# Optimization experiments

Hardware: AMD Instinct MI355X
Metric: run time of the kernel (lower is better)

## Reference

```python
import jax, jax.numpy as jnp
import numpy as np

B, T, E, R, A, M = 64, 2000, 512, 1024, 512, 8


def setup_inputs() -> dict:
    key = jax.random.key(0)
    ks = jax.random.split(key, 9)
    attention_hidden_state = jax.random.normal(ks[0], (B, R), dtype=jnp.float32)
    memory = jax.random.normal(ks[1], (B, T, E), dtype=jnp.float32)
    previous_location = jax.random.uniform(ks[2], (B, 1, M), dtype=jnp.float32) * 10.0
    mask = jnp.zeros((B, T), dtype=bool)
    # F = Linear(R->A, bias, xavier tanh) -> Linear(A->A, no bias, xavier tanh) -> tanh -> lin(A->3M, bias)
    g = 5.0 / 3.0  # tanh gain
    lim1 = g * np.sqrt(6.0 / (R + A))
    W1 = jax.random.uniform(ks[3], (A, R), minval=-lim1, maxval=lim1, dtype=jnp.float32)
    b1 = jnp.zeros((A,), dtype=jnp.float32)
    lim2 = g * np.sqrt(6.0 / (A + A))
    W2 = jax.random.uniform(ks[4], (A, A), minval=-lim2, maxval=lim2, dtype=jnp.float32)
    lim3 = np.sqrt(1.0 / A)
    Wlin = jax.random.uniform(ks[5], (3 * M, A), minval=-lim3, maxval=lim3, dtype=jnp.float32) * 0.01
    blin = jax.random.uniform(ks[6], (3 * M,), minval=-lim3, maxval=lim3, dtype=jnp.float32) * 0.008 - 2.0
    return {"attention_hidden_state": attention_hidden_state, "memory": memory,
            "previous_location": previous_location, "mask": mask,
            "W1": W1, "b1": b1, "W2": W2, "Wlin": Wlin, "blin": blin}


def reference(attention_hidden_state, memory, previous_location, mask, W1, b1, W2, Wlin, blin):
    # normalize_attention_input=True
    h = jnp.tanh(attention_hidden_state)                       # (B, R)
    x = jnp.tanh((h @ W1.T + b1) @ W2.T)                       # (B, A) 2-layer variant
    y = (x @ Wlin.T + blin)[:, None, :]                        # (B, 1, 3M)
    m = y.shape[-1] // 3
    w, delta, scale = y[..., :m], y[..., m:2 * m], y[..., 2 * m:]
    delta = jax.nn.sigmoid(delta)                              # (B, 1, M)
    loc = previous_location + delta                            # (B, 1, M)
    scale = jax.nn.sigmoid(scale) * 2.0 + 1.0                  # (B, 1, M)
    pos = jnp.arange(memory.shape[1], dtype=memory.dtype)[None, :, None]  # (1, T, 1)
    d = loc - pos                                              # (B, T, M)
    z = 0.5 * (jax.lax.erf((d + 0.5) * scale) - jax.lax.erf((d - 0.5) * scale))
    wmix = jax.nn.sigmoid(w)[:, 0, :]                          # (B, M)
    alignment = jnp.einsum('btm,bm->bt', z, wmix)              # (B, T)
    alignment = jnp.where(mask, jnp.zeros((), alignment.dtype), alignment)  # score_mask_value=0
    attention_weights = jax.nn.softmax(alignment, axis=1)      # (B, T)
    attention_context = jnp.einsum('bt,bte->be', attention_weights, memory)  # (B, E)
    return attention_context, attention_weights, loc
```

## Files before the change

### kernel.cpp

```cpp
#include <hip/hip_runtime.h>
#include <math.h>

#define B 64
#define T 2000
#define E 512
#define R 1024
#define A 512
#define M 8

#define NCH 16
#define TCH (T / NCH)
#define NP  (NCH * 4)

typedef float nfloat4 __attribute__((ext_vector_type(4)));

__device__ __forceinline__ float sigmoidf_(float x) { return 1.0f / (1.0f + expf(-x)); }
__device__ __forceinline__ float dot4_(float4 a, float4 b) {
    return (a.x * b.x + a.y * b.y) + (a.z * b.z + a.w * b.w);
}

__global__ __launch_bounds__(512) void mlp_align_kernel(
    const float* __restrict__ ahs, const float* __restrict__ prev_loc,
    const unsigned char* __restrict__ mask,
    const float* __restrict__ W1, const float* __restrict__ b1,
    const float* __restrict__ W2, const float* __restrict__ Wlin,
    const float* __restrict__ blin,
    float* __restrict__ out_w,
    float* __restrict__ out_loc)
{
    __shared__ float sh_h[R];
    __shared__ float sh_t[A];
    __shared__ float sh_x[A];
    __shared__ float sh_y[3 * M];
    __shared__ float sh_wmix[M], sh_loc[M], sh_scale[M];
    __shared__ float sred[8];
    __shared__ float sbval;

    const int b = blockIdx.x;
    const int tid = threadIdx.x;
    const int wave = tid >> 6;
    const int lane = tid & 63;

    for (int k = tid; k < R; k += 512) sh_h[k] = tanhf(ahs[b * R + k]);
    __syncthreads();

    {
        const float4* h4 = (const float4*)sh_h;
        const float4 h0 = h4[lane], h1 = h4[lane + 64],
                     h2 = h4[lane + 128], h3 = h4[lane + 192];
        for (int j = 0; j < 64; j += 2) {
            const int ja = wave * 64 + j;
            const int jb = ja + 1;
            const float4* ra = (const float4*)(W1 + (size_t)ja * R);
            const float4* rb = (const float4*)(W1 + (size_t)jb * R);
            float4 a0 = ra[lane], a1 = ra[lane + 64], a2 = ra[lane + 128], a3 = ra[lane + 192];
            float4 c0 = rb[lane], c1 = rb[lane + 64], c2 = rb[lane + 128], c3 = rb[lane + 192];
            float accA = (dot4_(h0, a0) + dot4_(h1, a1)) + (dot4_(h2, a2) + dot4_(h3, a3));
            float accB = (dot4_(h0, c0) + dot4_(h1, c1)) + (dot4_(h2, c2) + dot4_(h3, c3));
#pragma unroll
            for (int off = 32; off > 0; off >>= 1) {
                accA += __shfl_down(accA, off);
                accB += __shfl_down(accB, off);
            }
            if (lane == 0) {
                sh_t[ja] = accA + b1[ja];
                sh_t[jb] = accB + b1[jb];
            }
        }
    }
    __syncthreads();

    {
        const float4* t4 = (const float4*)sh_t;
        const float4 t0 = t4[lane], t1 = t4[lane + 64];
        for (int j = 0; j < 64; j += 2) {
            const int ja = wave * 64 + j;
            const int jb = ja + 1;
            const float4* ra = (const float4*)(W2 + (size_t)ja * A);
            const float4* rb = (const float4*)(W2 + (size_t)jb * A);
            float4 a0 = ra[lane], a1 = ra[lane + 64];
            float4 c0 = rb[lane], c1 = rb[lane + 64];
            float accA = dot4_(t0, a0) + dot4_(t1, a1);
            float accB = dot4_(t0, c0) + dot4_(t1, c1);
#pragma unroll
            for (int off = 32; off > 0; off >>= 1) {
                accA += __shfl_down(accA, off);
                accB += __shfl_down(accB, off);
            }
            if (lane == 0) {
                sh_x[ja] = tanhf(accA);
                sh_x[jb] = tanhf(accB);
            }
        }
    }
    __syncthreads();

    if (tid < 16 * 3 * M) {
        const int i = tid >> 4;
        const int l16 = tid & 15;
        float s = 0.f;
        for (int k = l16; k < A; k += 16) s += sh_x[k] * Wlin[i * A + k];
        s += __shfl_down(s, 8, 16);
        s += __shfl_down(s, 4, 16);
        s += __shfl_down(s, 2, 16);
        s += __shfl_down(s, 1, 16);
        if (l16 == 0) sh_y[i] = s + blin[i];
    }
    __syncthreads();

    if (tid < M) {
        const int m = tid;
        const float delta = sigmoidf_(sh_y[M + m]);
        const float loc = prev_loc[b * M + m] + delta;
        sh_wmix[m]  = sigmoidf_(sh_y[m]);
        sh_loc[m]   = loc;
        sh_scale[m] = sigmoidf_(sh_y[2 * M + m]) * 2.0f + 1.0f;
        out_loc[b * M + m] = loc;
    }
    __syncthreads();

    float a[4];
    float lsum = 0.f;
#pragma unroll
    for (int i = 0; i < 4; ++i) {
        const int t = tid + i * 512;
        if (t < T) {
            const float tf = (float)t;
            float v = 0.f;
#pragma unroll
            for (int m = 0; m < M; ++m) {
                const float d = sh_loc[m] - tf;
                const float s = sh_scale[m];
                v += 0.5f * (erff((d + 0.5f) * s) - erff((d - 0.5f) * s)) * sh_wmix[m];
            }
            if (mask[b * T + t]) v = 0.f;
            a[i] = expf(v);
            lsum += a[i];
        } else {
            a[i] = 0.f;
        }
    }
#pragma unroll
    for (int off = 32; off > 0; off >>= 1) lsum += __shfl_down(lsum, off);
    if (lane == 0) sred[wave] = lsum;
    __syncthreads();
    if (tid == 0) {
        float s0 = 0.f;
        for (int i = 0; i < 8; ++i) s0 += sred[i];
        sbval = s0;
    }
    __syncthreads();
    const float inv = 1.0f / sbval;

#pragma unroll
    for (int i = 0; i < 4; ++i) {
        const int t = tid + i * 512;
        if (t < T) out_w[b * T + t] = a[i] * inv;
    }
}

__global__ __launch_bounds__(512) void context_partial_kernel(
    const float* __restrict__ memory,
    const float* __restrict__ w,
    float* __restrict__ partials)
{
    __shared__ float sh_w[TCH];

    const int b = blockIdx.x;
    const int chunk = blockIdx.y;
    const int tid = threadIdx.x;
    const int t0 = chunk * TCH;

    if (tid < TCH) sh_w[tid] = w[b * T + t0 + tid];
    __syncthreads();

    const int e4 = tid & 127;
    const int tp = tid >> 7;
    const nfloat4* mem4 = (const nfloat4*)(memory + (size_t)(b * T + t0) * E);

    float acc0 = 0.f, acc1 = 0.f, acc2 = 0.f, acc3 = 0.f;
#pragma unroll 4
    for (int t = tp; t < TCH; t += 4) {
        const float wv = sh_w[t];
        const nfloat4 mv = __builtin_nontemporal_load(&mem4[(size_t)t * (E / 4) + e4]);
        acc0 += wv * mv.x;
        acc1 += wv * mv.y;
        acc2 += wv * mv.z;
        acc3 += wv * mv.w;
    }

    nfloat4 accv = {acc0, acc1, acc2, acc3};
    nfloat4* dst = (nfloat4*)(partials + (((size_t)b * NCH + chunk) * 4 + tp) * E);
    dst[e4] = accv;
}

__global__ __launch_bounds__(256) void context_reduce_kernel(
    const float* __restrict__ partials,
    float* __restrict__ out_ctx)
{
    const int idx = blockIdx.x * 256 + threadIdx.x;
    const int b = idx >> 7;
    const int e4 = idx & 127;
    const float4* p = (const float4*)partials + (size_t)b * NP * (E / 4) + e4;
    float4 s = {0.f, 0.f, 0.f, 0.f};
#pragma unroll 8
    for (int c = 0; c < NP; ++c) {
        const float4 v = p[(size_t)c * (E / 4)];
        s.x += v.x; s.y += v.y; s.z += v.z; s.w += v.w;
    }
    ((float4*)out_ctx)[idx] = s;
}

extern "C" void kernel_launch(void* const* d_in, const int* in_sizes, int n_in,
                              void* d_out, int out_size, void* d_ws, size_t ws_size,
                              hipStream_t stream) {
    const float* ahs      = (const float*)d_in[0];
    const float* memory   = (const float*)d_in[1];
    const float* prev_loc = (const float*)d_in[2];
    const unsigned char* mask = (const unsigned char*)d_in[3];
    const float* W1   = (const float*)d_in[4];
    const float* b1   = (const float*)d_in[5];
    const float* W2   = (const float*)d_in[6];
    const float* Wlin = (const float*)d_in[7];
    const float* blin = (const float*)d_in[8];

    float* out = (float*)d_out;
    float* out_ctx = out;
    float* out_w   = out + B * E;
    float* out_loc = out + B * E + B * T;
    float* partials = (float*)d_ws;

    mlp_align_kernel<<<dim3(B), dim3(512), 0, stream>>>(
        ahs, prev_loc, mask, W1, b1, W2, Wlin, blin, out_w, out_loc);

    context_partial_kernel<<<dim3(B, NCH), dim3(512), 0, stream>>>(
        memory, out_w, partials);

    context_reduce_kernel<<<dim3((B * E / 4) / 256), dim3(256), 0, stream>>>(
        partials, out_ctx);
}
```

Before: 434.3 us.

## Split MLP into batched layer kernels that reuse weight rows across four batches

The single per-batch MLP+alignment kernel is split into separate layer1, layer2 and head/alignment kernels. The layer kernels process four batch rows per block over a 16x8 grid, so each W1/W2 row is loaded once per four batches and the work is spread over more blocks. Wave reductions now use DPP instructions instead of shuffles. This cuts the redundant per-batch weight traffic (W1 is 2 MB) and improves parallelism, at the cost of two extra kernel launches and workspace round trips.

```diff
diff --git a/kernel.cpp b/kernel.cpp
--- a/kernel.cpp
+++ b/kernel.cpp
@@ -19,92 +19,143 @@
     return (a.x * b.x + a.y * b.y) + (a.z * b.z + a.w * b.w);
 }
 
-__global__ __launch_bounds__(512) void mlp_align_kernel(
-    const float* __restrict__ ahs, const float* __restrict__ prev_loc,
+__device__ __forceinline__ float wave_sum64_(float v) {
+#define DPPA_(c) v += __int_as_float(__builtin_amdgcn_update_dpp(0, __float_as_int(v), c, 0xf, 0xf, false))
+    DPPA_(0x111);
+    DPPA_(0x112);
+    DPPA_(0x114);
+    DPPA_(0x118);
+    DPPA_(0x142);
+    DPPA_(0x143);
+#undef DPPA_
+    return __int_as_float(__builtin_amdgcn_readlane(__float_as_int(v), 63));
+}
+
+__global__ __launch_bounds__(512) void layer1_kernel(
+    const float* __restrict__ ahs, const float* __restrict__ W1,
+    const float* __restrict__ b1, float* __restrict__ tws)
+{
+    __shared__ float4 sh_h[4 * 256];
+
+    const int bq = blockIdx.x, jt = blockIdx.y;
+    const int tid = threadIdx.x;
+    const int wave = tid >> 6, lane = tid & 63;
+    const int b0 = bq * 4;
+
+#pragma unroll
+    for (int s = 0; s < 2; ++s) {
+        const int idx = tid + s * 512;
+        const int bb = idx >> 8, k4 = idx & 255;
+        float4 v = ((const float4*)(ahs + (size_t)(b0 + bb) * R))[k4];
+        v.x = tanhf(v.x); v.y = tanhf(v.y); v.z = tanhf(v.z); v.w = tanhf(v.w);
+        sh_h[idx] = v;
+    }
+    __syncthreads();
+
+    float4 h4[4][4];
+#pragma unroll
+    for (int bb = 0; bb < 4; ++bb)
+#pragma unroll
+        for (int p = 0; p < 4; ++p)
+            h4[bb][p] = sh_h[bb * 256 + p * 64 + lane];
+
+    const int jbase = jt * 64 + wave * 8;
+#pragma unroll
+    for (int jj = 0; jj < 8; ++jj) {
+        const int j = jbase + jj;
+        const float4* wr = (const float4*)(W1 + (size_t)j * R);
+        const float4 w0 = wr[lane], w1 = wr[64 + lane],
+                     w2 = wr[128 + lane], w3 = wr[192 + lane];
+        const float bias = b1[j];
+        float r[4];
+#pragma unroll
+        for (int bb = 0; bb < 4; ++bb) {
+            float acc = (dot4_(h4[bb][0], w0) + dot4_(h4[bb][1], w1)) +
+                        (dot4_(h4[bb][2], w2) + dot4_(h4[bb][3], w3));
+            r[bb] = wave_sum64_(acc);
+        }
+        if (lane == 0) {
+#pragma unroll
+            for (int bb = 0; bb < 4; ++bb)
+                tws[(size_t)(b0 + bb) * A + j] = r[bb] + bias;
+        }
+    }
+}
+
+__global__ __launch_bounds__(512) void layer2_kernel(
+    const float* __restrict__ tws, const float* __restrict__ W2,
+    float* __restrict__ xws)
+{
+    __shared__ float4 sh_t[4 * 128];
+
+    const int bq = blockIdx.x, jt = blockIdx.y;
+    const int tid = threadIdx.x;
+    const int wave = tid >> 6, lane = tid & 63;
+    const int b0 = bq * 4;
+
+    {
+        const int bb = tid >> 7, k4 = tid & 127;
+        sh_t[tid] = ((const float4*)(tws + (size_t)(b0 + bb) * A))[k4];
+    }
+    __syncthreads();
+
+    float4 t4[4][2];
+#pragma unroll
+    for (int bb = 0; bb < 4; ++bb)
+#pragma unroll
+        for (int p = 0; p < 2; ++p)
+            t4[bb][p] = sh_t[bb * 128 + p * 64 + lane];
+
+    const int jbase = jt * 64 + wave * 8;
+#pragma unroll
+    for (int jj = 0; jj < 8; ++jj) {
+        const int j = jbase + jj;
+        const float4* wr = (const float4*)(W2 + (size_t)j * A);
+        const float4 w0 = wr[lane], w1 = wr[64 + lane];
+        float r[4];
+#pragma unroll
+        for (int bb = 0; bb < 4; ++bb) {
+            float acc = dot4_(t4[bb][0], w0) + dot4_(t4[bb][1], w1);
+            r[bb] = wave_sum64_(acc);
+        }
+        if (lane == 0) {
+#pragma unroll
+            for (int bb = 0; bb < 4; ++bb)
+                xws[(size_t)(b0 + bb) * A + j] = tanhf(r[bb]);
+        }
+    }
+}
+
+__global__ __launch_bounds__(256) void head_align_kernel(
+    const float* __restrict__ xws, const float* __restrict__ prev_loc,
     const unsigned char* __restrict__ mask,
-    const float* __restrict__ W1, const float* __restrict__ b1,
-    const float* __restrict__ W2, const float* __restrict__ Wlin,
-    const float* __restrict__ blin,
+    const float* __restrict__ Wlin, const float* __restrict__ blin,
     float* __restrict__ out_w,
     float* __restrict__ out_loc)
 {
-    __shared__ float sh_h[R];
-    __shared__ float sh_t[A];
     __shared__ float sh_x[A];
     __shared__ float sh_y[3 * M];
     __shared__ float sh_wmix[M], sh_loc[M], sh_scale[M];
-    __shared__ float sred[8];
+    __shared__ float sred[4];
     __shared__ float sbval;
 
     const int b = blockIdx.x;
     const int tid = threadIdx.x;
-    const int wave = tid >> 6;
-    const int lane = tid & 63;
-
-    for (int k = tid; k < R; k += 512) sh_h[k] = tanhf(ahs[b * R + k]);
+    const int wave = tid >> 6, lane = tid & 63;
+
+    if (tid < 128) ((float4*)sh_x)[tid] = ((const float4*)(xws + (size_t)b * A))[tid];
     __syncthreads();
 
     {
-        const float4* h4 = (const float4*)sh_h;
-        const float4 h0 = h4[lane], h1 = h4[lane + 64],
-                     h2 = h4[lane + 128], h3 = h4[lane + 192];
-        for (int j = 0; j < 64; j += 2) {
-            const int ja = wave * 64 + j;
-            const int jb = ja + 1;
-            const float4* ra = (const float4*)(W1 + (size_t)ja * R);
-            const float4* rb = (const float4*)(W1 + (size_t)jb * R);
-            float4 a0 = ra[lane], a1 = ra[lane + 64], a2 = ra[lane + 128], a3 = ra[lane + 192];
-            float4 c0 = rb[lane], c1 = rb[lane + 64], c2 = rb[lane + 128], c3 = rb[lane + 192];
-            float accA = (dot4_(h0, a0) + dot4_(h1, a1)) + (dot4_(h2, a2) + dot4_(h3, a3));
-            float accB = (dot4_(h0, c0) + dot4_(h1, c1)) + (dot4_(h2, c2) + dot4_(h3, c3));
-#pragma unroll
-            for (int off = 32; off > 0; off >>= 1) {
-                accA += __shfl_down(accA, off);
-                accB += __shfl_down(accB, off);
-            }
-            if (lane == 0) {
-                sh_t[ja] = accA + b1[ja];
-                sh_t[jb] = accB + b1[jb];
-            }
-        }
-    }
-    __syncthreads();
-
-    {
-        const float4* t4 = (const float4*)sh_t;
-        const float4 t0 = t4[lane], t1 = t4[lane + 64];
-        for (int j = 0; j < 64; j += 2) {
-            const int ja = wave * 64 + j;
-            const int jb = ja + 1;
-            const float4* ra = (const float4*)(W2 + (size_t)ja * A);
-            const float4* rb = (const float4*)(W2 + (size_t)jb * A);
-            float4 a0 = ra[lane], a1 = ra[lane + 64];
-            float4 c0 = rb[lane], c1 = rb[lane + 64];
-            float accA = dot4_(t0, a0) + dot4_(t1, a1);
-            float accB = dot4_(t0, c0) + dot4_(t1, c1);
-#pragma unroll
-            for (int off = 32; off > 0; off >>= 1) {
-                accA += __shfl_down(accA, off);
-                accB += __shfl_down(accB, off);
-            }
-            if (lane == 0) {
-                sh_x[ja] = tanhf(accA);
-                sh_x[jb] = tanhf(accB);
-            }
-        }
-    }
-    __syncthreads();
-
-    if (tid < 16 * 3 * M) {
-        const int i = tid >> 4;
-        const int l16 = tid & 15;
-        float s = 0.f;
-        for (int k = l16; k < A; k += 16) s += sh_x[k] * Wlin[i * A + k];
-        s += __shfl_down(s, 8, 16);
-        s += __shfl_down(s, 4, 16);
-        s += __shfl_down(s, 2, 16);
-        s += __shfl_down(s, 1, 16);
-        if (l16 == 0) sh_y[i] = s + blin[i];
+        const int i = tid >> 3, l8 = tid & 7;
+        if (i < 3 * M) {
+            float s = 0.f;
+            for (int k = l8; k < A; k += 8) s += sh_x[k] * Wlin[i * A + k];
+            s += __shfl_down(s, 4, 8);
+            s += __shfl_down(s, 2, 8);
+            s += __shfl_down(s, 1, 8);
+            if (l8 == 0) sh_y[i] = s + blin[i];
+        }
     }
     __syncthreads();
 
@@ -119,11 +170,11 @@
     }
     __syncthreads();
 
-    float a[4];
+    float a[8];
     float lsum = 0.f;
 #pragma unroll
-    for (int i = 0; i < 4; ++i) {
-        const int t = tid + i * 512;
+    for (int i = 0; i < 8; ++i) {
+        const int t = tid + i * 256;
         if (t < T) {
             const float tf = (float)t;
             float v = 0.f;
@@ -140,21 +191,16 @@
             a[i] = 0.f;
         }
     }
-#pragma unroll
-    for (int off = 32; off > 0; off >>= 1) lsum += __shfl_down(lsum, off);
-    if (lane == 0) sred[wave] = lsum;
-    __syncthreads();
-    if (tid == 0) {
-        float s0 = 0.f;
-        for (int i = 0; i < 8; ++i) s0 += sred[i];
-        sbval = s0;
-    }
+    const float wsum = wave_sum64_(lsum);
+    if (lane == 0) sred[wave] = wsum;
+    __syncthreads();
+    if (tid == 0) sbval = (sred[0] + sred[1]) + (sred[2] + sred[3]);
     __syncthreads();
     const float inv = 1.0f / sbval;
 
 #pragma unroll
-    for (int i = 0; i < 4; ++i) {
-        const int t = tid + i * 512;
+    for (int i = 0; i < 8; ++i) {
+        const int t = tid + i * 256;
         if (t < T) out_w[b * T + t] = a[i] * inv;
     }
 }
@@ -228,14 +274,17 @@
     float* out_ctx = out;
     float* out_w   = out + B * E;
     float* out_loc = out + B * E + B * T;
+
     float* partials = (float*)d_ws;
-
-    mlp_align_kernel<<<dim3(B), dim3(512), 0, stream>>>(
-        ahs, prev_loc, mask, W1, b1, W2, Wlin, blin, out_w, out_loc);
-
+    float* tws = partials + (size_t)B * NP * E;
+    float* xws = tws + (size_t)B * A;
+
+    layer1_kernel<<<dim3(16, 8), dim3(512), 0, stream>>>(ahs, W1, b1, tws);
+    layer2_kernel<<<dim3(16, 8), dim3(512), 0, stream>>>(tws, W2, xws);
+    head_align_kernel<<<dim3(B), dim3(256), 0, stream>>>(
+        xws, prev_loc, mask, Wlin, blin, out_w, out_loc);
     context_partial_kernel<<<dim3(B, NCH), dim3(512), 0, stream>>>(
         memory, out_w, partials);
-
     context_reduce_kernel<<<dim3((B * E / 4) / 256), dim3(256), 0, stream>>>(
         partials, out_ctx);
 }
```

Measured after the change: 449.1 us. 1.03x slower.
